# Kernel tuning notes

Measured on AMD Instinct MI355X. Metric: run time of the kernel, lower is better.

## Reference

```python
import jax, jax.numpy as jnp
import numpy as np

ALPHA = 1.5      # entmax alpha (q parameter)
N_ITER = 50      # entmax-bisect iterations (entmax library default)
B, S, DM, H, HKV, HD = 1, 2048, 2048, 16, 4, 128
ROPE_THETA = 10000.0


def _entmax_p(x):
    """alpha-entmax along last axis via bisection on tau (matches entmax.EntmaxBisect)."""
    am1 = ALPHA - 1.0
    pw = 1.0 / am1
    X = x * am1
    d = x.shape[-1]
    max_val = jnp.max(X, axis=-1, keepdims=True)
    tau_lo = max_val - 1.0                      # _gp(1, alpha) = 1
    tau_hi = max_val - (1.0 / d) ** am1          # _gp(1/d, alpha)
    dm0 = tau_hi - tau_lo

    def body(i, carry):
        tau_lo, dm, tau_m = carry
        dm = dm * 0.5
        tau_m = tau_lo + dm
        p = jnp.maximum(X - tau_m, 0.0) ** pw
        f = jnp.sum(p, axis=-1, keepdims=True) - 1.0
        tau_lo = jnp.where(f >= 0, tau_m, tau_lo)
        return (tau_lo, dm, tau_m)

    tau_lo, dm, tau_m = jax.lax.fori_loop(0, N_ITER, body, (tau_lo, dm0, tau_lo))
    p = jnp.maximum(X - tau_m, 0.0) ** pw
    return p / jnp.sum(p, axis=-1, keepdims=True)  # ensure_sum_one


@jax.custom_vjp
def entmax_bisect(x):
    return _entmax_p(x)

def _emx_fwd(x):
    p = _entmax_p(x)
    return p, p

def _emx_bwd(p, g):
    # entmax library backward: gppr = p^(2-alpha) on support
    gppr = jnp.where(p > 0, p ** (2.0 - ALPHA), 0.0)
    dX = g * gppr
    q = jnp.sum(dX, axis=-1, keepdims=True) / jnp.sum(gppr, axis=-1, keepdims=True)
    return ((dX - q * gppr),)

entmax_bisect.defvjp(_emx_fwd, _emx_bwd)


def _rotate_half(x):
    x1, x2 = x[..., : HD // 2], x[..., HD // 2:]
    return jnp.concatenate([-x2, x1], axis=-1)


def setup_inputs() -> dict:
    key = jax.random.key(0)
    k1, k2, k3, k4, k5 = jax.random.split(key, 5)
    hidden_states = jax.random.normal(k1, (B, S, DM), dtype=jnp.float32)
    wq = jax.random.normal(k2, (H * HD, DM), dtype=jnp.float32) * 0.02
    wk = jax.random.normal(k3, (HKV * HD, DM), dtype=jnp.float32) * 0.02
    wv = jax.random.normal(k4, (HKV * HD, DM), dtype=jnp.float32) * 0.02
    wo = jax.random.normal(k5, (DM, H * HD), dtype=jnp.float32) * 0.02
    # real Llama RoPE position embeddings
    inv_freq = 1.0 / (ROPE_THETA ** (np.arange(0, HD, 2, dtype=np.float32) / HD))
    pos = np.arange(S, dtype=np.float32)
    freqs = pos[:, None] * inv_freq[None, :]          # [S, HD/2]
    emb = np.concatenate([freqs, freqs], axis=-1)     # [S, HD]
    cos = jnp.asarray(np.cos(emb))[None]              # [1, S, HD]
    sin = jnp.asarray(np.sin(emb))[None]
    return {"hidden_states": hidden_states, "cos": cos, "sin": sin,
            "wq": wq, "wk": wk, "wv": wv, "wo": wo}


def reference(hidden_states, cos, sin, wq, wk, wv, wo):
    b, s, _ = hidden_states.shape
    scaling = HD ** -0.5
    # QKV projections -> [B, H, S, HD]
    q = (hidden_states @ wq.T).reshape(b, s, H, HD).transpose(0, 2, 1, 3)
    k = (hidden_states @ wk.T).reshape(b, s, HKV, HD).transpose(0, 2, 1, 3)
    v = (hidden_states @ wv.T).reshape(b, s, HKV, HD).transpose(0, 2, 1, 3)
    # RoPE (cos/sin broadcast over head axis)
    c, sn = cos[:, None, :, :], sin[:, None, :, :]
    q = q * c + _rotate_half(q) * sn
    k = k * c + _rotate_half(k) * sn
    # GQA: repeat kv heads
    g = H // HKV
    k = jnp.repeat(k, g, axis=1)
    v = jnp.repeat(v, g, axis=1)
    scores = jnp.einsum('bhqd,bhkd->bhqk', q, k) * scaling
    causal = jnp.tril(jnp.ones((s, s), dtype=bool))
    scores = jnp.where(causal, scores, -jnp.inf)
    attn = entmax_bisect(scores)                      # [B, H, S, S]
    out = jnp.einsum('bhqk,bhkd->bhqd', attn, v)
    out = out.transpose(0, 2, 1, 3).reshape(b, s, H * HD)
    out = out @ wo.T
    return (out, attn)
```

## Files before the change

kernel.cpp:

```cpp
#include <hip/hip_runtime.h>

typedef __bf16 bf16;
typedef __bf16 bf16x4 __attribute__((ext_vector_type(4)));
typedef __bf16 bf16x8 __attribute__((ext_vector_type(8)));
typedef float f32x4 __attribute__((ext_vector_type(4)));
typedef float f32x2 __attribute__((ext_vector_type(2)));

#define S 2048
#define DM 2048
#define HD 128
#define H 16
#define NQKV 3072
#define NEWTON_ITERS 12

__device__ __forceinline__ void gl2lds16(const void* g, void* l) {
    __builtin_amdgcn_global_load_lds(
        (const __attribute__((address_space(1))) void*)g,
        (__attribute__((address_space(3))) void*)l, 16, 0, 0);
}

__device__ __forceinline__ void nt_store4(f32x4 v, float* p) {
    __builtin_nontemporal_store(v, (f32x4*)p);
}

template <int CTRL, int RM>
__device__ __forceinline__ float dpp_zero(float x) {
    return __builtin_bit_cast(float, __builtin_amdgcn_update_dpp(
        0, __builtin_bit_cast(int, x), CTRL, RM, 0xf, false));
}
template <int CTRL, int RM>
__device__ __forceinline__ float dpp_self(float x) {
    int xi = __builtin_bit_cast(int, x);
    return __builtin_bit_cast(float, __builtin_amdgcn_update_dpp(xi, xi, CTRL, RM, 0xf, false));
}
__device__ __forceinline__ float wave_bcast63(float x) {
    return __builtin_bit_cast(float, __builtin_amdgcn_readlane(__builtin_bit_cast(int, x), 63));
}
__device__ __forceinline__ float wave_sum(float x) {
    x += dpp_zero<0x111, 0xf>(x);
    x += dpp_zero<0x112, 0xf>(x);
    x += dpp_zero<0x114, 0xf>(x);
    x += dpp_zero<0x118, 0xf>(x);
    x += dpp_zero<0x142, 0xa>(x);
    x += dpp_zero<0x143, 0xc>(x);
    return wave_bcast63(x);
}
__device__ __forceinline__ float wave_fmax(float x) {
    x = fmaxf(x, dpp_self<0x111, 0xf>(x));
    x = fmaxf(x, dpp_self<0x112, 0xf>(x));
    x = fmaxf(x, dpp_self<0x114, 0xf>(x));
    x = fmaxf(x, dpp_self<0x118, 0xf>(x));
    x = fmaxf(x, dpp_self<0x142, 0xa>(x));
    x = fmaxf(x, dpp_self<0x143, 0xc>(x));
    return wave_bcast63(x);
}

__global__ void cvt_all(const float* __restrict__ hid, const float* __restrict__ wq,
                        const float* __restrict__ wk, const float* __restrict__ wv,
                        const float* __restrict__ wo, bf16* __restrict__ bh,
                        bf16* __restrict__ bqkv, bf16* __restrict__ bwo) {
    int i = blockIdx.x * blockDim.x + threadIdx.x;
    const float* src;
    bf16* dst;
    int off;
    if (i < 1048576) { src = hid; dst = bh; off = i; }
    else if (i < 2097152) { src = wq; dst = bqkv; off = i - 1048576; }
    else if (i < 2359296) { src = wk; dst = bqkv + 2048 * 2048; off = i - 2097152; }
    else if (i < 2621440) { src = wv; dst = bqkv + 2048 * 2048 + 512 * 2048; off = i - 2359296; }
    else { src = wo; dst = bwo; off = i - 2621440; }
    float4 f = ((const float4*)src)[off];
    bf16x4 o;
    o[0] = (bf16)f.x; o[1] = (bf16)f.y; o[2] = (bf16)f.z; o[3] = (bf16)f.w;
    ((bf16x4*)dst)[off] = o;
}

template <int BM, int BN>
__global__ __launch_bounds__(256) void gemm_bt(const bf16* __restrict__ A,
                                               const bf16* __restrict__ B,
                                               float* __restrict__ C, int Ndim, int K) {
    __shared__ bf16 As[BM * 32];
    __shared__ bf16 Bs[BN * 32];
    int m0 = blockIdx.x * BM, n0 = blockIdx.y * BN;
    int t = threadIdx.x;
    int l = t & 63, w = t >> 6;
    int lane16 = l & 15, quad = l >> 4;

    const bf16* Abase = A + (size_t)m0 * K;
    const bf16* Bbase = B + (size_t)n0 * K;

    constexpr int MI = BM / 32, NI = BN / 32;
    int wm = (w & 1) * (BM / 2), wn = (w >> 1) * (BN / 2);
    f32x4 acc[MI][NI];
#pragma unroll
    for (int i = 0; i < MI; i++)
#pragma unroll
        for (int j = 0; j < NI; j++) acc[i][j] = (f32x4){0.f, 0.f, 0.f, 0.f};

    constexpr int AG = BM * 4;
    constexpr int BG = BN * 4;

    for (int k0 = 0; k0 < K; k0 += 32) {
#pragma unroll
        for (int it = 0; it < AG / 256; it++) {
            int c = it * 256 + t;
            gl2lds16(Abase + (size_t)(c >> 2) * K + k0 + (c & 3) * 8, &As[(c - l) * 8]);
        }
#pragma unroll
        for (int it = 0; it < BG / 256; it++) {
            int c = it * 256 + t;
            gl2lds16(Bbase + (size_t)(c >> 2) * K + k0 + (c & 3) * 8, &Bs[(c - l) * 8]);
        }
        __syncthreads();
        bf16x8 af[MI], bfr[NI];
#pragma unroll
        for (int i = 0; i < MI; i++)
            af[i] = *(const bf16x8*)&As[(wm + i * 16 + lane16) * 32 + quad * 8];
#pragma unroll
        for (int j = 0; j < NI; j++)
            bfr[j] = *(const bf16x8*)&Bs[(wn + j * 16 + lane16) * 32 + quad * 8];
#pragma unroll
        for (int i = 0; i < MI; i++)
#pragma unroll
            for (int j = 0; j < NI; j++)
                acc[i][j] = __builtin_amdgcn_mfma_f32_16x16x32_bf16(af[i], bfr[j], acc[i][j], 0, 0, 0);
        __syncthreads();
    }
#pragma unroll
    for (int i = 0; i < MI; i++)
#pragma unroll
        for (int j = 0; j < NI; j++) {
            float* cp = C + (size_t)(m0 + wm + i * 16 + quad * 4) * Ndim + n0 + wn + j * 16 + lane16;
#pragma unroll
            for (int r = 0; r < 4; r++) cp[(size_t)r * Ndim] = acc[i][j][r];
        }
}

__global__ void rope_qk(const float* __restrict__ qkv, const float* __restrict__ cosb,
                        const float* __restrict__ sinb, bf16* __restrict__ qs,
                        bf16* __restrict__ kb) {
    int col = blockIdx.x * 256 + threadIdx.x;
    int s = blockIdx.y;
    const float* row = qkv + (size_t)s * NQKV;
    float v = row[col];
    if (col < DM) {
        int h = col >> 7, d = col & 127;
        float c = cosb[s * HD + d], sn = sinb[s * HD + d];
        float other = row[(h << 7) + ((d < 64) ? (d + 64) : (d - 64))];
        float rot = (d < 64) ? -other : other;
        float o = v * c + rot * sn;
        qs[((size_t)h * S + s) * HD + d] = (bf16)(o * 0.04419417382415922f);
    } else {
        int c2 = col - DM;
        int kv = c2 >> 7, d = c2 & 127;
        float c = cosb[s * HD + d], sn = sinb[s * HD + d];
        float other = row[DM + (kv << 7) + ((d < 64) ? (d + 64) : (d - 64))];
        float rot = (d < 64) ? -other : other;
        float o = v * c + rot * sn;
        kb[((size_t)kv * S + s) * HD + d] = (bf16)o;
    }
}

__global__ __launch_bounds__(256) void vtrans(const float* __restrict__ qkv, bf16* __restrict__ vT) {
    __shared__ bf16 tile[64][66];
    int s0 = blockIdx.x * 64, y0 = blockIdx.y * 64;
    int t = threadIdx.x;
    int ty = t & 63, tr = t >> 6;
#pragma unroll
    for (int i = 0; i < 16; i++) {
        int s = tr + i * 4;
        float v = qkv[(size_t)(s0 + s) * NQKV + 2560 + y0 + ty];
        tile[s][ty] = (bf16)v;
    }
    __syncthreads();
#pragma unroll
    for (int i = 0; i < 16; i++) {
        int y = tr + i * 4;
        vT[(size_t)(y0 + y) * S + s0 + ty] = tile[ty][y];
    }
}

template <int SEGS>
__device__ __forceinline__ void attn_body(const bf16* __restrict__ qs, const bf16* __restrict__ kb,
                                          const bf16* __restrict__ vT, float* __restrict__ attn,
                                          bf16* __restrict__ o, int r0, int h,
                                          float (&buf)[16][532]) {
    constexpr int NREG2 = SEGS * 4;
    int jlen = r0 + 16;
    int l = threadIdx.x & 63;
    int w = threadIdx.x >> 6;
    int lane16 = l & 15, quad = l >> 4;

    const bf16* qrow = qs + ((size_t)h * S + (r0 + lane16)) * HD + quad * 8;
    bf16x8 afrag[4];
#pragma unroll
    for (int kc = 0; kc < 4; kc++) afrag[kc] = *(const bf16x8*)(qrow + kc * 32);

    const bf16* kbase = kb + (size_t)(h >> 2) * S * HD;
    const bf16* vbase = vT + (size_t)(h >> 2) * HD * S;
    f32x2 xr[NREG2];

#pragma unroll
    for (int sgi = 0; sgi < SEGS; sgi++) {
        int j0 = sgi * 512;
        float (*sb)[532] = buf;
#pragma unroll
        for (int tt = 0; tt < 2; tt++) {
            int t = w + tt * 16;
            int jt = j0 + t * 16;
            if (jt < jlen) {
                f32x4 acc = {0.f, 0.f, 0.f, 0.f};
                const bf16* kp = kbase + (size_t)(jt + lane16) * HD + quad * 8;
#pragma unroll
                for (int kc = 0; kc < 4; kc++) {
                    bf16x8 b = *(const bf16x8*)(kp + kc * 32);
                    acc = __builtin_amdgcn_mfma_f32_16x16x32_bf16(afrag[kc], b, acc, 0, 0, 0);
                }
                if (jt + 15 > r0) {
                    int jj = jt + lane16;
#pragma unroll
                    for (int r = 0; r < 4; r++) {
                        int rowi = quad * 4 + r;
                        float v = acc[r];
                        if (jj > r0 + rowi) v = -1e30f;
                        sb[rowi][t * 16 + lane16] = v;
                    }
                } else {
#pragma unroll
                    for (int r = 0; r < 4; r++) sb[quad * 4 + r][t * 16 + lane16] = acc[r];
                }
            }
        }
        __syncthreads();
#pragma unroll
        for (int part = 0; part < 2; part++) {
            float4 fq = *(const float4*)&sb[w][part * 256 + l * 4];
            if (sgi == SEGS - 1) {
                int jb = j0 + part * 256 + l * 4;
                xr[sgi * 4 + part * 2 + 0] =
                    (f32x2){(jb + 0 < jlen) ? fq.x : -1e30f, (jb + 1 < jlen) ? fq.y : -1e30f};
                xr[sgi * 4 + part * 2 + 1] =
                    (f32x2){(jb + 2 < jlen) ? fq.z : -1e30f, (jb + 3 < jlen) ? fq.w : -1e30f};
            } else {
                xr[sgi * 4 + part * 2 + 0] = (f32x2){fq.x, fq.y};
                xr[sgi * 4 + part * 2 + 1] = (f32x2){fq.z, fq.w};
            }
        }
        __syncthreads();
    }

    float* arow = attn + ((size_t)h * S + (r0 + w)) * S;

    {
        f32x4 z4 = {0.f, 0.f, 0.f, 0.f};
        for (int j = SEGS * 512 + l * 4; j < S; j += 256) nt_store4(z4, &arow[j]);
    }

    const f32x2 z2 = {0.f, 0.f};
    float mx = -1e30f;
#pragma unroll
    for (int c = 0; c < NREG2; c++) mx = fmaxf(mx, fmaxf(xr[c][0], xr[c][1]));
    float m = wave_fmax(mx);

    float tau = m - 1.0f;
#pragma unroll 1
    for (int it = 0; it < NEWTON_ITERS; it++) {
        f32x2 tvi = {tau, tau};
        f32x2 fa = z2, fb = z2, ga = z2, gb = z2;
#pragma unroll
        for (int c = 0; c < NREG2; c += 2) {
            f32x2 t0 = __builtin_elementwise_max(xr[c] - tvi, z2);
            fa += t0 * t0; ga += t0;
            f32x2 t1 = __builtin_elementwise_max(xr[c + 1] - tvi, z2);
            fb += t1 * t1; gb += t1;
        }
        f32x2 fv = fa + fb, gv = ga + gb;
        float f = wave_sum(fv[0] + fv[1]);
        float g = wave_sum(gv[0] + gv[1]);
        tau += (f - 1.0f) / (2.0f * g + 1e-20f);
    }

    f32x2 tv = {tau, tau};
    float inv;
    {
        f32x2 sa = z2, sbv = z2;
#pragma unroll
        for (int c = 0; c < NREG2; c += 2) {
            f32x2 t0 = __builtin_elementwise_max(xr[c] - tv, z2);
            sa += t0 * t0;
            f32x2 t1 = __builtin_elementwise_max(xr[c + 1] - tv, z2);
            sbv += t1 * t1;
        }
        f32x2 sv = sa + sbv;
        float ssum = wave_sum(sv[0] + sv[1]);
        inv = 1.0f / ssum;
    }

    int jt_o = (w & 7) * 16;
    int kh = (w >> 3) * 256;
    f32x4 acc_o = {0.f, 0.f, 0.f, 0.f};
    f32x2 inv2 = {inv, inv};

    __syncthreads();
#pragma unroll
    for (int sgi = 0; sgi < SEGS; sgi++) {
        int j0 = sgi * 512;
        bf16 (*pbf)[552] = (bf16(*)[552])(&buf[0][0]);
#pragma unroll
        for (int part = 0; part < 2; part++) {
            f32x2 ta = __builtin_elementwise_max(xr[sgi * 4 + part * 2 + 0] - tv, z2);
            f32x2 tb = __builtin_elementwise_max(xr[sgi * 4 + part * 2 + 1] - tv, z2);
            f32x2 pa = (ta * ta) * inv2;
            f32x2 pb = (tb * tb) * inv2;
            f32x4 pv = {pa[0], pa[1], pb[0], pb[1]};
            nt_store4(pv, &arow[j0 + part * 256 + l * 4]);
            bf16x4 pbv;
            pbv[0] = (bf16)pv[0]; pbv[1] = (bf16)pv[1];
            pbv[2] = (bf16)pv[2]; pbv[3] = (bf16)pv[3];
            *(bf16x4*)&pbf[w][part * 256 + l * 4] = pbv;
        }
        __syncthreads();
#pragma unroll
        for (int ks = 0; ks < 8; ks++) {
            int kk = kh + ks * 32;
            bf16x8 a = *(const bf16x8*)&pbf[lane16][kk + quad * 8];
            bf16x8 b = *(const bf16x8*)(vbase + (size_t)(jt_o + lane16) * S + j0 + kk + quad * 8);
            acc_o = __builtin_amdgcn_mfma_f32_16x16x32_bf16(a, b, acc_o, 0, 0, 0);
        }
        __syncthreads();
    }

    if (w >= 8) {
#pragma unroll
        for (int r = 0; r < 4; r++) buf[w - 8][l * 4 + r] = acc_o[r];
    }
    __syncthreads();
    if (w < 8) {
        bf16* op = o + (size_t)(r0 + quad * 4) * DM + h * HD + jt_o + lane16;
#pragma unroll
        for (int r = 0; r < 4; r++) {
            float v = acc_o[r] + buf[w][l * 4 + r];
            op[(size_t)r * DM] = (bf16)v;
        }
    }
}

__global__ __launch_bounds__(1024, 8) void attn_av_all(const bf16* __restrict__ qs,
                                                       const bf16* __restrict__ kb,
                                                       const bf16* __restrict__ vT,
                                                       float* __restrict__ attn,
                                                       bf16* __restrict__ o) {
    __shared__ float buf[16][532];
    int b = blockIdx.x;
    int h = b & 15;
    int qh = b >> 4;
    attn_body<4>(qs, kb, vT, attn, o, (96 + qh) * 16, h, buf);
    __syncthreads();
    attn_body<3>(qs, kb, vT, attn, o, (64 + qh) * 16, h, buf);
    __syncthreads();
    attn_body<2>(qs, kb, vT, attn, o, (32 + qh) * 16, h, buf);
    __syncthreads();
    attn_body<1>(qs, kb, vT, attn, o, qh * 16, h, buf);
}

extern "C" void kernel_launch(void* const* d_in, const int* in_sizes, int n_in,
                              void* d_out, int out_size, void* d_ws, size_t ws_size,
                              hipStream_t stream) {
    const float* hidden = (const float*)d_in[0];
    const float* cosb   = (const float*)d_in[1];
    const float* sinb   = (const float*)d_in[2];
    const float* wq     = (const float*)d_in[3];
    const float* wk     = (const float*)d_in[4];
    const float* wv     = (const float*)d_in[5];
    const float* wo     = (const float*)d_in[6];
    char* ws = (char*)d_ws;
    bf16*  bf_hidden = (bf16*)(ws);
    bf16*  bf_wqkv   = (bf16*)(ws + 8388608);
    bf16*  bf_wo     = (bf16*)(ws + 20971520);
    float* qkv_raw   = (float*)(ws + 29360128);
    bf16*  qsb       = (bf16*)(ws + 54525952);
    bf16*  kbb       = (bf16*)(ws + 62914560);
    bf16*  vTb       = (bf16*)(ws + 65011712);
    float* out  = (float*)d_out;
    float* attn = out + 4194304;

    cvt_all<<<dim3(14336), 256, 0, stream>>>(hidden, wq, wk, wv, wo, bf_hidden, bf_wqkv, bf_wo);

    gemm_bt<64, 128><<<dim3(32, 24), 256, 0, stream>>>(bf_hidden, bf_wqkv, qkv_raw, NQKV, DM);

    rope_qk<<<dim3(10, S), 256, 0, stream>>>(qkv_raw, cosb, sinb, qsb, kbb);
    vtrans<<<dim3(32, 8), 256, 0, stream>>>(qkv_raw, vTb);

    attn_av_all<<<dim3(512), 1024, 0, stream>>>(qsb, kbb, vTb, attn, bf_hidden);

    gemm_bt<64, 128><<<dim3(32, 16), 256, 0, stream>>>(bf_hidden, bf_wo, out, DM, DM);
}
```

Before: 588.8 us.

## Double-buffer P tile in LDS and defer attention-probability stores after AV

The bf16 probability tile in LDS now alternates between two halves of the shared buffer, one per segment, with the row stride padded to 556. This removes the trailing barrier in each AV segment loop and the barrier before it. The fp32 attention-probability global stores and the zero-fill of the masked tail move to after the AV matmul and output write, recomputing p from registers. The intent is to keep MFMA work from waiting behind the large nontemporal store stream, at the cost of recomputing the probabilities once more. Launch bounds are restated with explicit flat-workgroup-size and waves-per-EU attributes.

New measurement: 601.4 us. 1.02x slower.

```diff
diff --git a/kernel.cpp b/kernel.cpp
--- a/kernel.cpp
+++ b/kernel.cpp
@@ -12,6 +12,7 @@
 #define H 16
 #define NQKV 3072
 #define NEWTON_ITERS 12
+#define BROW 556
 
 __device__ __forceinline__ void gl2lds16(const void* g, void* l) {
     __builtin_amdgcn_global_load_lds(
@@ -183,7 +184,7 @@
 __device__ __forceinline__ void attn_body(const bf16* __restrict__ qs, const bf16* __restrict__ kb,
                                           const bf16* __restrict__ vT, float* __restrict__ attn,
                                           bf16* __restrict__ o, int r0, int h,
-                                          float (&buf)[16][532]) {
+                                          float (&buf)[16][BROW]) {
     constexpr int NREG2 = SEGS * 4;
     int jlen = r0 + 16;
     int l = threadIdx.x & 63;
@@ -202,7 +203,7 @@
 #pragma unroll
     for (int sgi = 0; sgi < SEGS; sgi++) {
         int j0 = sgi * 512;
-        float (*sb)[532] = buf;
+        float (*sb)[BROW] = buf;
 #pragma unroll
         for (int tt = 0; tt < 2; tt++) {
             int t = w + tt * 16;
@@ -248,13 +249,6 @@
         __syncthreads();
     }
 
-    float* arow = attn + ((size_t)h * S + (r0 + w)) * S;
-
-    {
-        f32x4 z4 = {0.f, 0.f, 0.f, 0.f};
-        for (int j = SEGS * 512 + l * 4; j < S; j += 256) nt_store4(z4, &arow[j]);
-    }
-
     const f32x2 z2 = {0.f, 0.f};
     float mx = -1e30f;
 #pragma unroll
@@ -300,35 +294,32 @@
     f32x4 acc_o = {0.f, 0.f, 0.f, 0.f};
     f32x2 inv2 = {inv, inv};
 
-    __syncthreads();
 #pragma unroll
     for (int sgi = 0; sgi < SEGS; sgi++) {
         int j0 = sgi * 512;
-        bf16 (*pbf)[552] = (bf16(*)[552])(&buf[0][0]);
+        bf16 (*pb)[BROW] = (bf16(*)[BROW])(&buf[0][0]) + (sgi & 1) * 16;
 #pragma unroll
         for (int part = 0; part < 2; part++) {
             f32x2 ta = __builtin_elementwise_max(xr[sgi * 4 + part * 2 + 0] - tv, z2);
             f32x2 tb = __builtin_elementwise_max(xr[sgi * 4 + part * 2 + 1] - tv, z2);
             f32x2 pa = (ta * ta) * inv2;
-            f32x2 pb = (tb * tb) * inv2;
-            f32x4 pv = {pa[0], pa[1], pb[0], pb[1]};
-            nt_store4(pv, &arow[j0 + part * 256 + l * 4]);
+            f32x2 pb2 = (tb * tb) * inv2;
             bf16x4 pbv;
-            pbv[0] = (bf16)pv[0]; pbv[1] = (bf16)pv[1];
-            pbv[2] = (bf16)pv[2]; pbv[3] = (bf16)pv[3];
-            *(bf16x4*)&pbf[w][part * 256 + l * 4] = pbv;
+            pbv[0] = (bf16)pa[0]; pbv[1] = (bf16)pa[1];
+            pbv[2] = (bf16)pb2[0]; pbv[3] = (bf16)pb2[1];
+            *(bf16x4*)&pb[w][part * 256 + l * 4] = pbv;
         }
         __syncthreads();
 #pragma unroll
         for (int ks = 0; ks < 8; ks++) {
             int kk = kh + ks * 32;
-            bf16x8 a = *(const bf16x8*)&pbf[lane16][kk + quad * 8];
+            bf16x8 a = *(const bf16x8*)&pb[lane16][kk + quad * 8];
             bf16x8 b = *(const bf16x8*)(vbase + (size_t)(jt_o + lane16) * S + j0 + kk + quad * 8);
             acc_o = __builtin_amdgcn_mfma_f32_16x16x32_bf16(a, b, acc_o, 0, 0, 0);
         }
-        __syncthreads();
-    }
-
+    }
+
+    __syncthreads();
     if (w >= 8) {
 #pragma unroll
         for (int r = 0; r < 4; r++) buf[w - 8][l * 4 + r] = acc_o[r];
@@ -342,14 +333,32 @@
             op[(size_t)r * DM] = (bf16)v;
         }
     }
-}
-
-__global__ __launch_bounds__(1024, 8) void attn_av_all(const bf16* __restrict__ qs,
-                                                       const bf16* __restrict__ kb,
-                                                       const bf16* __restrict__ vT,
-                                                       float* __restrict__ attn,
-                                                       bf16* __restrict__ o) {
-    __shared__ float buf[16][532];
+
+    float* arow = attn + ((size_t)h * S + (r0 + w)) * S;
+#pragma unroll
+    for (int sgi = 0; sgi < SEGS; sgi++) {
+        int j0 = sgi * 512;
+#pragma unroll
+        for (int part = 0; part < 2; part++) {
+            f32x2 ta = __builtin_elementwise_max(xr[sgi * 4 + part * 2 + 0] - tv, z2);
+            f32x2 tb = __builtin_elementwise_max(xr[sgi * 4 + part * 2 + 1] - tv, z2);
+            f32x2 pa = (ta * ta) * inv2;
+            f32x2 pb2 = (tb * tb) * inv2;
+            f32x4 pv = {pa[0], pa[1], pb2[0], pb2[1]};
+            nt_store4(pv, &arow[j0 + part * 256 + l * 4]);
+        }
+    }
+    f32x4 z4 = {0.f, 0.f, 0.f, 0.f};
+    for (int j = SEGS * 512 + l * 4; j < S; j += 256) nt_store4(z4, &arow[j]);
+}
+
+__global__ __attribute__((amdgpu_flat_work_group_size(1024, 1024), amdgpu_waves_per_eu(8)))
+void attn_av_all(const bf16* __restrict__ qs,
+                 const bf16* __restrict__ kb,
+                 const bf16* __restrict__ vT,
+                 float* __restrict__ attn,
+                 bf16* __restrict__ o) {
+    __shared__ float buf[16][BROW];
     int b = blockIdx.x;
     int h = b & 15;
     int qh = b >> 4;
```
